# Kernel optimization log

Measured on AMD Instinct MI355X. Metric: run time of the kernel, lower is better.

Reference implementation:

```python
import jax, jax.numpy as jnp
import numpy as np

MANIFOLD_DIM = 256
EPS = 1e-8

def quaternion_normalize(q):
    # q: (..., 4) -> unit quaternions
    return q / (jnp.linalg.norm(q, axis=-1, keepdims=True) + EPS)

def quaternion_mul(a, b):
    # Hamilton product, broadcasting over leading dims. a, b: (..., 4)
    aw, ax, ay, az = a[..., 0], a[..., 1], a[..., 2], a[..., 3]
    bw, bx, by, bz = b[..., 0], b[..., 1], b[..., 2], b[..., 3]
    return jnp.stack([
        aw * bw - ax * bx - ay * by - az * bz,
        aw * bx + ax * bw + ay * bz - az * by,
        aw * by - ax * bz + ay * bw + az * bx,
        aw * bz + ax * by - ay * bx + az * bw,
    ], axis=-1)

def compute_berry_phase(path):
    # path: (B, N, 4). gamma = 2*acos(Re(q0*q1*...*q_{N-1}*q0))
    path = quaternion_normalize(path)
    # ordered product via log-depth parallel scan (quaternion mul is associative)
    prod_all = jax.lax.associative_scan(quaternion_mul, path, axis=1)[:, -1]  # (B, 4)
    prod = quaternion_mul(prod_all, path[:, 0])
    return 2.0 * jnp.arccos(jnp.clip(prod[..., 0], -1.0, 1.0))  # (B,)

def holomorphic_audit(q_state):
    # torch.gradient(t)[0] == gradient along dim 0 (batch axis), unit spacing.
    # dw+dx+dy+dz == gradient of the component-sum (linearity of gradient).
    df = jnp.abs(jnp.gradient(q_state.sum(axis=-1), axis=0))  # (B, N)
    res = jnp.mean(df)
    return res < 0.05, res

def _to_quaternion(x):
    B = x.shape[0]
    return x.reshape(B, -1, 4)

def setup_inputs() -> dict:
    key = jax.random.key(0)
    ks = jax.random.split(key, 9)
    B, HW, L, G, D = 8, 4096, 8192, 4096, MANIFOLD_DIM
    s = 0.05  # keep latents small so Berry product stays numerically tame
    return {
        "vision_data": jax.random.normal(ks[0], (B, HW, 3), jnp.float32),
        "text_data": jax.random.normal(ks[1], (B, L, 1), jnp.float32),
        "genomic_data": jax.random.normal(ks[2], (B, G, 4), jnp.float32),
        "Wv": jax.random.normal(ks[3], (3, D), jnp.float32) * s,
        "bv": jax.random.normal(ks[4], (D,), jnp.float32) * s,
        "Wt": jax.random.normal(ks[5], (1, D), jnp.float32) * s,
        "bt": jax.random.normal(ks[6], (D,), jnp.float32) * s,
        "Wg": jax.random.normal(ks[7], (4, D), jnp.float32) * s,
        "bg": jax.random.normal(ks[8], (D,), jnp.float32) * s,
    }

def reference(vision_data, text_data, genomic_data, Wv, bv, Wt, bt, Wg, bg):
    v_lat = vision_data @ Wv + bv      # (B, HW, 256)
    t_lat = text_data @ Wt + bt        # (B, L, 256)
    g_lat = genomic_data @ Wg + bg     # (B, G, 256)
    v_path = _to_quaternion(v_lat)     # (B, HW*64, 4)
    t_path = _to_quaternion(t_lat)
    g_path = _to_quaternion(g_lat)
    phi_v = compute_berry_phase(v_path)
    phi_t = compute_berry_phase(t_path)
    phi_g = compute_berry_phase(g_path)
    interference = jnp.abs(phi_v.mean() - phi_t.mean())
    genomic_invariant_score = jnp.exp(-jnp.abs(phi_g - interference))  # (B,)
    _, res_v = holomorphic_audit(v_path)
    _, res_t = holomorphic_audit(t_path)
    return genomic_invariant_score, interference, res_v, res_t
```

## Files before the change

kernel.cpp:

```cpp
#include <hip/hip_runtime.h>
#include <math.h>

#define BB 8
#define HW 4096
#define LTXT 8192
#define GG 4096
#define DD 256


typedef float v2f __attribute__((ext_vector_type(2)));
#define VFMA __builtin_elementwise_fma

__device__ __forceinline__ v2f vsplat(float s) { v2f r; r.x = s; r.y = s; return r; }

struct QF { float w, x, y, z; };
struct QP { v2f w, x, y, z; };

__device__ __forceinline__ QF qmulf(const QF a, const QF b) {
    QF r;
    r.w = fmaf(a.w, b.w, -fmaf(a.x, b.x, fmaf(a.y, b.y, a.z * b.z)));
    r.x = fmaf(a.w, b.x, fmaf(a.x, b.w, fmaf(a.y, b.z, -(a.z * b.y))));
    r.y = fmaf(a.w, b.y, fmaf(a.y, b.w, fmaf(a.z, b.x, -(a.x * b.z))));
    r.z = fmaf(a.w, b.z, fmaf(a.x, b.y, fmaf(a.z, b.w, -(a.y * b.x))));
    return r;
}

__device__ __forceinline__ QP qmulp(const QP a, const QP b) {
    QP r;
    r.w = VFMA(a.w, b.w, -VFMA(a.x, b.x, VFMA(a.y, b.y, a.z * b.z)));
    r.x = VFMA(a.w, b.x, VFMA(a.x, b.w, VFMA(a.y, b.z, -(a.z * b.y))));
    r.y = VFMA(a.w, b.y, VFMA(a.y, b.w, VFMA(a.z, b.x, -(a.x * b.z))));
    r.z = VFMA(a.w, b.z, VFMA(a.x, b.y, VFMA(a.z, b.w, -(a.y * b.x))));
    return r;
}

__device__ __forceinline__ QF wave_ordered_prod(QF p, int lane) {
    #pragma unroll
    for (int s = 1; s < 64; s <<= 1) {
        QF o;
        o.w = __shfl_xor(p.w, s, 64);
        o.x = __shfl_xor(p.x, s, 64);
        o.y = __shfl_xor(p.y, s, 64);
        o.z = __shfl_xor(p.z, s, 64);
        const bool hi = (lane & s) != 0;
        QF a = hi ? o : p;
        QF b = hi ? p : o;
        p = qmulf(a, b);
    }
    return p;
}

__device__ __forceinline__ QP wave_ordered_prod_p(QP p, int lane) {
    #pragma unroll
    for (int s = 1; s < 64; s <<= 1) {
        QP o;
        o.w.x = __shfl_xor(p.w.x, s, 64); o.w.y = __shfl_xor(p.w.y, s, 64);
        o.x.x = __shfl_xor(p.x.x, s, 64); o.x.y = __shfl_xor(p.x.y, s, 64);
        o.y.x = __shfl_xor(p.y.x, s, 64); o.y.y = __shfl_xor(p.y.y, s, 64);
        o.z.x = __shfl_xor(p.z.x, s, 64); o.z.y = __shfl_xor(p.z.y, s, 64);
        const bool hi = (lane & s) != 0;
        QP a, b;
        a.w = hi ? o.w : p.w; a.x = hi ? o.x : p.x; a.y = hi ? o.y : p.y; a.z = hi ? o.z : p.z;
        b.w = hi ? p.w : o.w; b.x = hi ? p.x : o.x; b.y = hi ? p.y : o.y; b.z = hi ? p.z : o.z;
        p = qmulp(a, b);
    }
    return p;
}

template<int K, int BQ>
__device__ __forceinline__ void chain_pair(
    const float* __restrict__ X, const float* __restrict__ W,
    const float* __restrict__ bias, int rowBase,
    float* __restrict__ out4, float* sprod)
{
    constexpr int V = K + 1;
    constexpr int NB = 64 / BQ;
    const int t = threadIdx.x;
    const int rA = rowBase + t;
    const int rB = rA + 128;

    v2f xv[K];
    #pragma unroll
    for (int k = 0; k < K; ++k) {
        xv[k].x = X[(size_t)rA * K + k];
        xv[k].y = X[(size_t)rB * K + k];
    }

    float4 A[BQ * V], Bb[BQ * V];
    QP p;
    float MA = 1.0f, MB = 1.0f, rrA = 0.0f, rrB = 0.0f;

    auto LOADB = [&](float4* dst, int bidx) {
        const float* bb = bias + 4 * (bidx * BQ);
        const float* wb = W + 4 * (bidx * BQ);
        #pragma unroll
        for (int j = 0; j < BQ; ++j) {
            dst[j * V + 0] = *(const float4*)(bb + 4 * j);
            #pragma unroll
            for (int k = 0; k < K; ++k)
                dst[j * V + 1 + k] = *(const float4*)(wb + k * DD + 4 * j);
        }
    };

    auto COMPUTE = [&](const float4* src, int bidx) {
        QP pb; v2f tt;
        #pragma unroll
        for (int j = 0; j < BQ; ++j) {
            const float4 b4 = src[j * V + 0];
            v2f l0 = vsplat(b4.x), l1 = vsplat(b4.y), l2 = vsplat(b4.z), l3 = vsplat(b4.w);
            #pragma unroll
            for (int k = 0; k < K; ++k) {
                const float4 w4 = src[j * V + 1 + k];
                l0 = VFMA(xv[k], vsplat(w4.x), l0);
                l1 = VFMA(xv[k], vsplat(w4.y), l1);
                l2 = VFMA(xv[k], vsplat(w4.z), l2);
                l3 = VFMA(xv[k], vsplat(w4.w), l3);
            }
            const v2f n2 = VFMA(l0, l0, VFMA(l1, l1, VFMA(l2, l2, l3 * l3)));
            rrA += __builtin_amdgcn_rsqf(n2.x);
            rrB += __builtin_amdgcn_rsqf(n2.y);
            QP q; q.w = l0; q.x = l1; q.y = l2; q.z = l3;
            if (j == 0) { pb = q; tt = n2; }
            else        { pb = qmulp(pb, q); tt *= n2; }
        }
        const int e2A = ((__float_as_int(tt.x) >> 23) - 127) >> 1;
        const int e2B = ((__float_as_int(tt.y) >> 23) - 127) >> 1;
        const float scA = __int_as_float((127 - e2A) << 23);
        const float scB = __int_as_float((127 - e2B) << 23);
        MA *= tt.x * (scA * scA);
        MB *= tt.y * (scB * scB);
        v2f sc; sc.x = scA; sc.y = scB;
        pb.w *= sc; pb.x *= sc; pb.y *= sc; pb.z *= sc;
        if (bidx == 0) p = pb;
        else           p = qmulp(p, pb);
    };

    LOADB(A, 0);
    for (int gg = 0; gg < NB / 2; ++gg) {
        LOADB(Bb, 2 * gg + 1);
        COMPUTE(A, 2 * gg);
        const int nb = (2 * gg + 2 < NB) ? (2 * gg + 2) : (NB - 1);
        LOADB(A, nb);
        COMPUTE(Bb, 2 * gg + 1);
    }

    {
        const float invA = 1.0f / (sqrtf(MA) * fmaf(1e-8f, rrA, 1.0f));
        const float invB = 1.0f / (sqrtf(MB) * fmaf(1e-8f, rrB, 1.0f));
        v2f iv; iv.x = invA; iv.y = invB;
        p.w *= iv; p.x *= iv; p.y *= iv; p.z *= iv;
    }

    const int lane = t & 63;
    p = wave_ordered_prod_p(p, lane);

    const int w = t >> 6;
    if (lane == 0) {
        float* s8 = sprod + w * 8;
        s8[0] = p.w.x; s8[1] = p.x.x; s8[2] = p.y.x; s8[3] = p.z.x;
        s8[4] = p.w.y; s8[5] = p.x.y; s8[6] = p.y.y; s8[7] = p.z.y;
    }
    __syncthreads();
    if (t == 0) {
        QF A0 = { sprod[0], sprod[1], sprod[2], sprod[3] };
        QF A1 = { sprod[8], sprod[9], sprod[10], sprod[11] };
        QF B0 = { sprod[4], sprod[5], sprod[6], sprod[7] };
        QF B1 = { sprod[12], sprod[13], sprod[14], sprod[15] };
        QF r = qmulf(qmulf(qmulf(A0, A1), B0), B1);
        float4 outv = { r.w, r.x, r.y, r.z };
        *(float4*)out4 = outv;
    }
}

__global__ __launch_bounds__(128) void worker_kernel(
    const float* __restrict__ vis, const float* __restrict__ txt, const float* __restrict__ gen,
    const float* __restrict__ Wv, const float* __restrict__ bv,
    const float* __restrict__ Wt, const float* __restrict__ bt,
    const float* __restrict__ Wg, const float* __restrict__ bg,
    float* __restrict__ wsf, double* __restrict__ dws)
{
    __shared__ double sred[128];
    float* sprod = (float*)sred;

    const int t  = threadIdx.x;
    const int id = blockIdx.x;

    if (id < 128) {
        const int b = id >> 4, chunk = id & 15;
        chain_pair<3, 4>(vis + (size_t)b * HW * 3, Wv, bv, chunk * 256,
                         wsf + (size_t)id * 4, sprod);
    } else if (id < 384) {
        const int i2 = id - 128;
        const int b = i2 >> 5, chunk = i2 & 31;
        chain_pair<1, 4>(txt + (size_t)b * LTXT, Wt, bt, chunk * 256,
                         wsf + 512 + (size_t)i2 * 4, sprod);
    } else if (id < 512) {
        const int i2 = id - 384;
        const int b = i2 >> 4, chunk = i2 & 15;
        chain_pair<4, 2>(gen + (size_t)b * GG * 4, Wg, bg, chunk * 256,
                         wsf + 1536 + (size_t)i2 * 4, sprod);
    } else if (id < 544) {
        const int aid = id - 512;
        const int r = aid * 128 + t;
        float gx[8], gy[8], gz[8];
        {
            float vx[8], vy[8], vz[8];
            #pragma unroll
            for (int b = 0; b < 8; ++b) {
                const size_t base = ((size_t)b * HW + r) * 3;
                vx[b] = vis[base]; vy[b] = vis[base+1]; vz[b] = vis[base+2];
            }
            #pragma unroll
            for (int b = 0; b < 8; ++b) {
                if (b == 0)      { gx[b] = vx[1]-vx[0];  gy[b] = vy[1]-vy[0];  gz[b] = vz[1]-vz[0]; }
                else if (b == 7) { gx[b] = vx[7]-vx[6];  gy[b] = vy[7]-vy[6];  gz[b] = vz[7]-vz[6]; }
                else             { gx[b] = (vx[b+1]-vx[b-1])*0.5f; gy[b] = (vy[b+1]-vy[b-1])*0.5f; gz[b] = (vz[b+1]-vz[b-1])*0.5f; }
            }
        }
        double acc = 0.0;
        #pragma unroll 4
        for (int i = 0; i < 64; ++i) {
            const float4 a0 = *(const float4*)(Wv + 4*i);
            const float4 a1 = *(const float4*)(Wv + DD + 4*i);
            const float4 a2 = *(const float4*)(Wv + 2*DD + 4*i);
            const float wq0 = a0.x + a0.y + a0.z + a0.w;
            const float wq1 = a1.x + a1.y + a1.z + a1.w;
            const float wq2 = a2.x + a2.y + a2.z + a2.w;
            float acc8 = 0.0f;
            #pragma unroll
            for (int b = 0; b < 8; ++b)
                acc8 += fabsf(fmaf(gx[b], wq0, fmaf(gy[b], wq1, gz[b] * wq2)));
            acc += (double)acc8;
        }
        sred[t] = acc;
        __syncthreads();
        for (int off = 64; off > 0; off >>= 1) {
            if (t < off) sred[t] += sred[t + off];
            __syncthreads();
        }
        if (t == 0) dws[aid] = sred[0];
    } else {
        const int aid = id - 544;
        const int l = aid * 128 + t;
        float tv[8];
        #pragma unroll
        for (int b = 0; b < 8; ++b) tv[b] = txt[(size_t)b * LTXT + l];
        double acc = 0.0;
        #pragma unroll
        for (int b = 0; b < 8; ++b) {
            float gb;
            if (b == 0)      gb = tv[1] - tv[0];
            else if (b == 7) gb = tv[7] - tv[6];
            else             gb = (tv[b+1] - tv[b-1]) * 0.5f;
            acc += (double)fabsf(gb);
        }
        sred[t] = acc;
        __syncthreads();
        for (int off = 64; off > 0; off >>= 1) {
            if (t < off) sred[t] += sred[t + off];
            __syncthreads();
        }
        if (t == 0) dws[32 + aid] = sred[0];
    }
}

__global__ __launch_bounds__(256) void finalize_kernel(
    const float* __restrict__ vis, const float* __restrict__ txt, const float* __restrict__ gen,
    const float* __restrict__ Wv, const float* __restrict__ bv,
    const float* __restrict__ Wt, const float* __restrict__ bt,
    const float* __restrict__ Wg, const float* __restrict__ bg,
    const float* __restrict__ wsf, const double* __restrict__ dws,
    float* __restrict__ out)
{
    __shared__ float sphi[24];
    __shared__ double sred[256];
    __shared__ double s_sumv, s_sumt, s_sumw;
    const int t = threadIdx.x;
    const int lane = t & 63, w = t >> 6;

    #pragma unroll
    for (int j = 0; j < 6; ++j) {
        const int pair = w * 6 + j;
        const int m = pair >> 3, b = pair & 7;
        const int nch = (m == 1) ? 32 : 16;
        const float* base = wsf + ((m == 0) ? 0 : (m == 1) ? 512 : 1536) + (size_t)b * nch * 4;
        QF p = { 1.0f, 0.0f, 0.0f, 0.0f };
        if (lane < nch) {
            const float4 c0 = *(const float4*)(base + lane * 4);
            p = { c0.x, c0.y, c0.z, c0.w };
        }
        p = wave_ordered_prod(p, lane);
        if (lane == 0) {
            float lat[4];
            if (m == 0) {
                const float x0 = vis[(size_t)b*HW*3], x1 = vis[(size_t)b*HW*3+1], x2 = vis[(size_t)b*HW*3+2];
                #pragma unroll
                for (int c = 0; c < 4; ++c)
                    lat[c] = fmaf(x0, Wv[c], fmaf(x1, Wv[DD+c], fmaf(x2, Wv[2*DD+c], bv[c])));
            } else if (m == 1) {
                const float x0 = txt[(size_t)b*LTXT];
                #pragma unroll
                for (int c = 0; c < 4; ++c) lat[c] = fmaf(x0, Wt[c], bt[c]);
            } else {
                const float x0 = gen[(size_t)b*GG*4], x1 = gen[(size_t)b*GG*4+1],
                            x2 = gen[(size_t)b*GG*4+2], x3 = gen[(size_t)b*GG*4+3];
                #pragma unroll
                for (int c = 0; c < 4; ++c)
                    lat[c] = fmaf(x0, Wg[c], fmaf(x1, Wg[DD+c], fmaf(x2, Wg[2*DD+c], fmaf(x3, Wg[3*DD+c], bg[c]))));
            }
            const float n = sqrtf(fmaf(lat[0], lat[0], fmaf(lat[1], lat[1], fmaf(lat[2], lat[2], lat[3] * lat[3]))));
            const float inv = 1.0f / (n + 1e-8f);
            QF q0 = { lat[0]*inv, lat[1]*inv, lat[2]*inv, lat[3]*inv };
            p = qmulf(p, q0);
            float ww = p.w;
            ww = fminf(1.0f, fmaxf(-1.0f, ww));
            sphi[pair] = 2.0f * acosf(ww);
        }
    }
    __syncthreads();

    sred[t] = (t < 32) ? dws[t] : 0.0; __syncthreads();
    for (int off = 128; off > 0; off >>= 1) { if (t < off) sred[t] += sred[t+off]; __syncthreads(); }
    if (t == 0) s_sumv = sred[0];
    __syncthreads();

    sred[t] = (t < 64) ? dws[32 + t] : 0.0; __syncthreads();
    for (int off = 128; off > 0; off >>= 1) { if (t < off) sred[t] += sred[t+off]; __syncthreads(); }
    if (t == 0) s_sumt = sred[0];
    __syncthreads();

    double aw = 0.0;
    if (t < 64) {
        const int d0 = 4 * t;
        aw = (double)fabsf(Wt[d0] + Wt[d0+1] + Wt[d0+2] + Wt[d0+3]);
    }
    sred[t] = aw; __syncthreads();
    for (int off = 128; off > 0; off >>= 1) { if (t < off) sred[t] += sred[t+off]; __syncthreads(); }
    if (t == 0) s_sumw = sred[0];
    __syncthreads();

    if (t == 0) {
        float mv = 0.0f, mt = 0.0f;
        for (int b = 0; b < 8; ++b) { mv += sphi[b]; mt += sphi[8 + b]; }
        mv *= 0.125f; mt *= 0.125f;
        const float interf = fabsf(mv - mt);
        for (int b = 0; b < 8; ++b)
            out[b] = expf(-fabsf(sphi[16 + b] - interf));
        out[8]  = interf;
        out[9]  = (float)(s_sumv / 2097152.0);
        out[10] = (float)(s_sumt * s_sumw / 4194304.0);
    }
}

extern "C" void kernel_launch(void* const* d_in, const int* in_sizes, int n_in,
                              void* d_out, int out_size, void* d_ws, size_t ws_size,
                              hipStream_t stream) {
    (void)in_sizes; (void)n_in; (void)out_size; (void)ws_size;
    const float* vis = (const float*)d_in[0];
    const float* txt = (const float*)d_in[1];
    const float* gen = (const float*)d_in[2];
    const float* Wv  = (const float*)d_in[3];
    const float* bv  = (const float*)d_in[4];
    const float* Wt  = (const float*)d_in[5];
    const float* bt  = (const float*)d_in[6];
    const float* Wg  = (const float*)d_in[7];
    const float* bg  = (const float*)d_in[8];
    float*  wsf = (float*)d_ws;
    double* dws = (double*)((char*)d_ws + 65536);
    float*  out = (float*)d_out;

    hipLaunchKernelGGL(worker_kernel, dim3(608), dim3(128), 0, stream,
                       vis, txt, gen, Wv, bv, Wt, bt, Wg, bg, wsf, dws);
    hipLaunchKernelGGL(finalize_kernel, dim3(1), dim3(256), 0, stream,
                       vis, txt, gen, Wv, bv, Wt, bt, Wg, bg, wsf, dws, out);
}
```

Baseline: 30.43 us.

## Split each row chain across two waves over quaternion halves, doubling block count

Each block now handles 128 rows instead of 256. Its two waves split the 64 quaternions per row into two halves of 32, and the halves are combined via shared memory before a single wave-level ordered product. This halves the serial per-thread chain length and doubles the grid to fill more CUs. In exchange it adds an LDS exchange of a full wave of quaternions, twice as many partial products for the finalize kernel, and full unrolling of the load/compute loop, which raises register pressure.

```diff
diff --git a/kernel.cpp b/kernel.cpp
--- a/kernel.cpp
+++ b/kernel.cpp
@@ -68,16 +68,19 @@
 }
 
 template<int K, int BQ>
-__device__ __forceinline__ void chain_pair(
+__device__ __forceinline__ void chain_hp(
     const float* __restrict__ X, const float* __restrict__ W,
     const float* __restrict__ bias, int rowBase,
-    float* __restrict__ out4, float* sprod)
+    float* __restrict__ out4, float* __restrict__ sprod )
 {
     constexpr int V = K + 1;
-    constexpr int NB = 64 / BQ;
+    constexpr int NB = 32 / BQ;
     const int t = threadIdx.x;
-    const int rA = rowBase + t;
-    const int rB = rA + 128;
+    const int lane = t & 63;
+    const int h = t >> 6;
+    const int rA = rowBase + lane;
+    const int rB = rA + 64;
+    const int i0 = h * 32;
 
     v2f xv[K];
     #pragma unroll
@@ -91,8 +94,9 @@
     float MA = 1.0f, MB = 1.0f, rrA = 0.0f, rrB = 0.0f;
 
     auto LOADB = [&](float4* dst, int bidx) {
-        const float* bb = bias + 4 * (bidx * BQ);
-        const float* wb = W + 4 * (bidx * BQ);
+        const int q0 = i0 + bidx * BQ;
+        const float* bb = bias + 4 * q0;
+        const float* wb = W + 4 * q0;
         #pragma unroll
         for (int j = 0; j < BQ; ++j) {
             dst[j * V + 0] = *(const float4*)(bb + 4 * j);
@@ -136,6 +140,7 @@
     };
 
     LOADB(A, 0);
+    #pragma unroll
     for (int gg = 0; gg < NB / 2; ++gg) {
         LOADB(Bb, 2 * gg + 1);
         COMPUTE(A, 2 * gg);
@@ -151,24 +156,26 @@
         p.w *= iv; p.x *= iv; p.y *= iv; p.z *= iv;
     }
 
-    const int lane = t & 63;
-    p = wave_ordered_prod_p(p, lane);
-
-    const int w = t >> 6;
-    if (lane == 0) {
-        float* s8 = sprod + w * 8;
+    if (h == 1) {
+        float* s8 = sprod + lane * 8;
         s8[0] = p.w.x; s8[1] = p.x.x; s8[2] = p.y.x; s8[3] = p.z.x;
         s8[4] = p.w.y; s8[5] = p.x.y; s8[6] = p.y.y; s8[7] = p.z.y;
     }
     __syncthreads();
-    if (t == 0) {
-        QF A0 = { sprod[0], sprod[1], sprod[2], sprod[3] };
-        QF A1 = { sprod[8], sprod[9], sprod[10], sprod[11] };
-        QF B0 = { sprod[4], sprod[5], sprod[6], sprod[7] };
-        QF B1 = { sprod[12], sprod[13], sprod[14], sprod[15] };
-        QF r = qmulf(qmulf(qmulf(A0, A1), B0), B1);
-        float4 outv = { r.w, r.x, r.y, r.z };
-        *(float4*)out4 = outv;
+    if (h == 0) {
+        const float* s8 = sprod + lane * 8;
+        QP o;
+        o.w.x = s8[0]; o.x.x = s8[1]; o.y.x = s8[2]; o.z.x = s8[3];
+        o.w.y = s8[4]; o.x.y = s8[5]; o.y.y = s8[6]; o.z.y = s8[7];
+        p = qmulp(p, o);
+        p = wave_ordered_prod_p(p, lane);
+        if (lane == 0) {
+            QF a = { p.w.x, p.x.x, p.y.x, p.z.x };
+            QF b = { p.w.y, p.x.y, p.y.y, p.z.y };
+            QF r = qmulf(a, b);
+            float4 outv = { r.w, r.x, r.y, r.z };
+            *(float4*)out4 = outv;
+        }
     }
 }
 
@@ -179,28 +186,29 @@
     const float* __restrict__ Wg, const float* __restrict__ bg,
     float* __restrict__ wsf, double* __restrict__ dws)
 {
-    __shared__ double sred[128];
-    float* sprod = (float*)sred;
+    __shared__ double sbuf[256];
+    float* sprod = (float*)sbuf;
+    double* sred = sbuf;
 
     const int t  = threadIdx.x;
     const int id = blockIdx.x;
 
-    if (id < 128) {
-        const int b = id >> 4, chunk = id & 15;
-        chain_pair<3, 4>(vis + (size_t)b * HW * 3, Wv, bv, chunk * 256,
-                         wsf + (size_t)id * 4, sprod);
-    } else if (id < 384) {
-        const int i2 = id - 128;
+    if (id < 256) {
+        const int b = id >> 5, chunk = id & 31;
+        chain_hp<3, 4>(vis + (size_t)b * HW * 3, Wv, bv, chunk * 128,
+                       wsf + (size_t)id * 4, sprod);
+    } else if (id < 768) {
+        const int i2 = id - 256;
+        const int b = i2 >> 6, chunk = i2 & 63;
+        chain_hp<1, 4>(txt + (size_t)b * LTXT, Wt, bt, chunk * 128,
+                       wsf + 1024 + (size_t)i2 * 4, sprod);
+    } else if (id < 1024) {
+        const int i2 = id - 768;
         const int b = i2 >> 5, chunk = i2 & 31;
-        chain_pair<1, 4>(txt + (size_t)b * LTXT, Wt, bt, chunk * 256,
-                         wsf + 512 + (size_t)i2 * 4, sprod);
-    } else if (id < 512) {
-        const int i2 = id - 384;
-        const int b = i2 >> 4, chunk = i2 & 15;
-        chain_pair<4, 2>(gen + (size_t)b * GG * 4, Wg, bg, chunk * 256,
-                         wsf + 1536 + (size_t)i2 * 4, sprod);
-    } else if (id < 544) {
-        const int aid = id - 512;
+        chain_hp<4, 2>(gen + (size_t)b * GG * 4, Wg, bg, chunk * 128,
+                       wsf + 3072 + (size_t)i2 * 4, sprod);
+    } else if (id < 1056) {
+        const int aid = id - 1024;
         const int r = aid * 128 + t;
         float gx[8], gy[8], gz[8];
         {
@@ -240,7 +248,7 @@
         }
         if (t == 0) dws[aid] = sred[0];
     } else {
-        const int aid = id - 544;
+        const int aid = id - 1056;
         const int l = aid * 128 + t;
         float tv[8];
         #pragma unroll
@@ -282,8 +290,8 @@
     for (int j = 0; j < 6; ++j) {
         const int pair = w * 6 + j;
         const int m = pair >> 3, b = pair & 7;
-        const int nch = (m == 1) ? 32 : 16;
-        const float* base = wsf + ((m == 0) ? 0 : (m == 1) ? 512 : 1536) + (size_t)b * nch * 4;
+        const int nch = (m == 1) ? 64 : 32;
+        const float* base = wsf + ((m == 0) ? 0 : (m == 1) ? 1024 : 3072) + (size_t)b * nch * 4;
         QF p = { 1.0f, 0.0f, 0.0f, 0.0f };
         if (lane < nch) {
             const float4 c0 = *(const float4*)(base + lane * 4);
@@ -369,7 +377,7 @@
     double* dws = (double*)((char*)d_ws + 65536);
     float*  out = (float*)d_out;
 
-    hipLaunchKernelGGL(worker_kernel, dim3(608), dim3(128), 0, stream,
+    hipLaunchKernelGGL(worker_kernel, dim3(1120), dim3(128), 0, stream,
                        vis, txt, gen, Wv, bv, Wt, bt, Wg, bg, wsf, dws);
     hipLaunchKernelGGL(finalize_kernel, dim3(1), dim3(256), 0, stream,
                        vis, txt, gen, Wv, bv, Wt, bt, Wg, bg, wsf, dws, out);
```

New measurement: 33.25 us. 9.3% more time.

## Split quaternion chain into two independent halves for more ILP

Applied to the files above, without the earlier changes.

Each thread now runs the 64-quaternion ordered product as two independent 32-quaternion chains, halves 0 and 1, and multiplies them together at the end. The two dependent qmul chains can interleave, which is meant to hide FMA and rsq latency. The launch bound now requests a minimum of one block per CU and the vision block size drops from 4 to 2, so more registers are available per thread. In exchange, register pressure rises and occupancy may fall.

```diff
diff --git a/kernel.cpp b/kernel.cpp
--- a/kernel.cpp
+++ b/kernel.cpp
@@ -68,13 +68,13 @@
 }
 
 template<int K, int BQ>
-__device__ __forceinline__ void chain_pair(
+__device__ __forceinline__ void chain_dual(
     const float* __restrict__ X, const float* __restrict__ W,
     const float* __restrict__ bias, int rowBase,
-    float* __restrict__ out4, float* sprod)
+    float* __restrict__ out4, float* __restrict__ sprod)
 {
     constexpr int V = K + 1;
-    constexpr int NB = 64 / BQ;
+    constexpr int NB2 = 32 / BQ;
     const int t = threadIdx.x;
     const int rA = rowBase + t;
     const int rB = rA + 128;
@@ -86,13 +86,15 @@
         xv[k].y = X[(size_t)rB * K + k];
     }
 
-    float4 A[BQ * V], Bb[BQ * V];
-    QP p;
-    float MA = 1.0f, MB = 1.0f, rrA = 0.0f, rrB = 0.0f;
-
-    auto LOADB = [&](float4* dst, int bidx) {
-        const float* bb = bias + 4 * (bidx * BQ);
-        const float* wb = W + 4 * (bidx * BQ);
+    float4 A0[BQ * V], B0[BQ * V], A1[BQ * V], B1[BQ * V];
+    QP p0, p1;
+    float M0A = 1.0f, M0B = 1.0f, rr0A = 0.0f, rr0B = 0.0f;
+    float M1A = 1.0f, M1B = 1.0f, rr1A = 0.0f, rr1B = 0.0f;
+
+    auto LOADB = [&](float4* dst, int half, int bidx) {
+        const int q0 = half * 32 + bidx * BQ;
+        const float* bb = bias + 4 * q0;
+        const float* wb = W + 4 * q0;
         #pragma unroll
         for (int j = 0; j < BQ; ++j) {
             dst[j * V + 0] = *(const float4*)(bb + 4 * j);
@@ -102,7 +104,8 @@
         }
     };
 
-    auto COMPUTE = [&](const float4* src, int bidx) {
+    auto COMPUTE = [&](const float4* src, QP& p, float& MA, float& MB,
+                       float& rrA, float& rrB, int bidx) {
         QP pb; v2f tt;
         #pragma unroll
         for (int j = 0; j < BQ; ++j) {
@@ -135,21 +138,27 @@
         else           p = qmulp(p, pb);
     };
 
-    LOADB(A, 0);
-    for (int gg = 0; gg < NB / 2; ++gg) {
-        LOADB(Bb, 2 * gg + 1);
-        COMPUTE(A, 2 * gg);
-        const int nb = (2 * gg + 2 < NB) ? (2 * gg + 2) : (NB - 1);
-        LOADB(A, nb);
-        COMPUTE(Bb, 2 * gg + 1);
+    LOADB(A0, 0, 0); LOADB(A1, 1, 0);
+    for (int gg = 0; gg < NB2 / 2; ++gg) {
+        LOADB(B0, 0, 2 * gg + 1); LOADB(B1, 1, 2 * gg + 1);
+        COMPUTE(A0, p0, M0A, M0B, rr0A, rr0B, 2 * gg);
+        COMPUTE(A1, p1, M1A, M1B, rr1A, rr1B, 2 * gg);
+        const int nb = (2 * gg + 2 < NB2) ? (2 * gg + 2) : (NB2 - 1);
+        LOADB(A0, 0, nb); LOADB(A1, 1, nb);
+        COMPUTE(B0, p0, M0A, M0B, rr0A, rr0B, 2 * gg + 1);
+        COMPUTE(B1, p1, M1A, M1B, rr1A, rr1B, 2 * gg + 1);
     }
 
     {
-        const float invA = 1.0f / (sqrtf(MA) * fmaf(1e-8f, rrA, 1.0f));
-        const float invB = 1.0f / (sqrtf(MB) * fmaf(1e-8f, rrB, 1.0f));
-        v2f iv; iv.x = invA; iv.y = invB;
-        p.w *= iv; p.x *= iv; p.y *= iv; p.z *= iv;
-    }
+        v2f iv0, iv1;
+        iv0.x = 1.0f / (sqrtf(M0A) * fmaf(1e-8f, rr0A, 1.0f));
+        iv0.y = 1.0f / (sqrtf(M0B) * fmaf(1e-8f, rr0B, 1.0f));
+        iv1.x = 1.0f / (sqrtf(M1A) * fmaf(1e-8f, rr1A, 1.0f));
+        iv1.y = 1.0f / (sqrtf(M1B) * fmaf(1e-8f, rr1B, 1.0f));
+        p0.w *= iv0; p0.x *= iv0; p0.y *= iv0; p0.z *= iv0;
+        p1.w *= iv1; p1.x *= iv1; p1.y *= iv1; p1.z *= iv1;
+    }
+    QP p = qmulp(p0, p1);
 
     const int lane = t & 63;
     p = wave_ordered_prod_p(p, lane);
@@ -162,17 +171,17 @@
     }
     __syncthreads();
     if (t == 0) {
-        QF A0 = { sprod[0], sprod[1], sprod[2], sprod[3] };
-        QF A1 = { sprod[8], sprod[9], sprod[10], sprod[11] };
-        QF B0 = { sprod[4], sprod[5], sprod[6], sprod[7] };
-        QF B1 = { sprod[12], sprod[13], sprod[14], sprod[15] };
-        QF r = qmulf(qmulf(qmulf(A0, A1), B0), B1);
+        QF A0q = { sprod[0], sprod[1], sprod[2], sprod[3] };
+        QF A1q = { sprod[8], sprod[9], sprod[10], sprod[11] };
+        QF B0q = { sprod[4], sprod[5], sprod[6], sprod[7] };
+        QF B1q = { sprod[12], sprod[13], sprod[14], sprod[15] };
+        QF r = qmulf(qmulf(qmulf(A0q, A1q), B0q), B1q);
         float4 outv = { r.w, r.x, r.y, r.z };
         *(float4*)out4 = outv;
     }
 }
 
-__global__ __launch_bounds__(128) void worker_kernel(
+__global__ __launch_bounds__(128, 1) void worker_kernel(
     const float* __restrict__ vis, const float* __restrict__ txt, const float* __restrict__ gen,
     const float* __restrict__ Wv, const float* __restrict__ bv,
     const float* __restrict__ Wt, const float* __restrict__ bt,
@@ -187,17 +196,17 @@
 
     if (id < 128) {
         const int b = id >> 4, chunk = id & 15;
-        chain_pair<3, 4>(vis + (size_t)b * HW * 3, Wv, bv, chunk * 256,
+        chain_dual<3, 2>(vis + (size_t)b * HW * 3, Wv, bv, chunk * 256,
                          wsf + (size_t)id * 4, sprod);
     } else if (id < 384) {
         const int i2 = id - 128;
         const int b = i2 >> 5, chunk = i2 & 31;
-        chain_pair<1, 4>(txt + (size_t)b * LTXT, Wt, bt, chunk * 256,
+        chain_dual<1, 4>(txt + (size_t)b * LTXT, Wt, bt, chunk * 256,
                          wsf + 512 + (size_t)i2 * 4, sprod);
     } else if (id < 512) {
         const int i2 = id - 384;
         const int b = i2 >> 4, chunk = i2 & 15;
-        chain_pair<4, 2>(gen + (size_t)b * GG * 4, Wg, bg, chunk * 256,
+        chain_dual<4, 2>(gen + (size_t)b * GG * 4, Wg, bg, chunk * 256,
                          wsf + 1536 + (size_t)i2 * 4, sprod);
     } else if (id < 544) {
         const int aid = id - 512;
```

After: 33.02 us. 1.09x slower.
